# Performance work log

Measured on AMD Instinct MI355X. Metric: run time of the kernel, lower is better.

The kernel has to match this reference:

```python
import jax, jax.numpy as jnp
import numpy as np

H = 8            # num_heads
EPS = 1e-5       # LayerNorm eps (torch default)
SLOPE = 0.01     # leaky_relu negative slope (torch default)


def layernorm(x, g, b):
    mu = jnp.mean(x, axis=-1, keepdims=True)
    var = jnp.mean((x - mu) ** 2, axis=-1, keepdims=True)
    return (x - mu) * jax.lax.rsqrt(var + EPS) * g + b


def setup_inputs() -> dict:
    key = jax.random.key(0)
    ks = jax.random.split(key, 20)
    B, T, Din, Dh = 4, 2048, 512, 512
    s_in = 1.0 / np.sqrt(Din)
    s_h = 1.0 / np.sqrt(Dh)
    inp = {
        'q': jax.random.normal(ks[0], (B, T, Din), jnp.float32),
        'k': jax.random.normal(ks[1], (B, T, Din), jnp.float32),
        'v': jax.random.normal(ks[2], (B, T, Din), jnp.float32),
        # attention projections (stored as [in, out] for x @ W + b)
        'Wq': jax.random.uniform(ks[3], (Din, Dh), jnp.float32, -s_in, s_in),
        'bq': jax.random.uniform(ks[4], (Dh,), jnp.float32, -s_in, s_in),
        'Wk': jax.random.uniform(ks[5], (Din, Dh), jnp.float32, -s_in, s_in),
        'bk': jax.random.uniform(ks[6], (Dh,), jnp.float32, -s_in, s_in),
        'Wv': jax.random.uniform(ks[7], (Din, Dh), jnp.float32, -s_in, s_in),
        'bv': jax.random.uniform(ks[8], (Dh,), jnp.float32, -s_in, s_in),
        'Wo': jax.random.uniform(ks[9], (Dh, Dh), jnp.float32, -s_h, s_h),
        'bo': jax.random.uniform(ks[10], (Dh,), jnp.float32, -s_h, s_h),
        # FFN
        'Wh': jax.random.uniform(ks[11], (Dh, Dh), jnp.float32, -s_h, s_h),
        'bh': jax.random.uniform(ks[12], (Dh,), jnp.float32, -s_h, s_h),
        'W2': jax.random.uniform(ks[13], (Dh, Dh), jnp.float32, -s_h, s_h),
        'b2': jax.random.uniform(ks[14], (Dh,), jnp.float32, -s_h, s_h),
        # LayerNorms
        'g1': jnp.ones((Dh,), jnp.float32),
        'be1': jnp.zeros((Dh,), jnp.float32),
        'g2': jnp.ones((Dh,), jnp.float32),
        'be2': jnp.zeros((Dh,), jnp.float32),
    }
    return inp


def _block(q, k, v, Wq, bq, Wk, bk, Wv, bv, Wo, bo, Wh, bh, W2, b2, g1, be1, g2, be2):
    B, Tq, _ = q.shape
    Tk = k.shape[1]
    Dh = Wq.shape[1]
    dh = Dh // H
    # projections -> [B, H, T, dh]
    qh = (q @ Wq + bq).reshape(B, Tq, H, dh).transpose(0, 2, 1, 3)
    kh = (k @ Wk + bk).reshape(B, Tk, H, dh).transpose(0, 2, 1, 3)
    vh = (v @ Wv + bv).reshape(B, Tk, H, dh).transpose(0, 2, 1, 3)
    scores = jnp.einsum('bhqd,bhkd->bhqk', qh, kh) / np.sqrt(dh)
    # causal mask: tril with diagonal = Tk - Tq (matches get_causal_mask)
    mask = jnp.tril(jnp.ones((Tq, Tk), bool), k=Tk - Tq)
    scores = jnp.where(mask, scores, -jnp.inf)
    attn = jax.nn.softmax(scores, axis=-1)
    x = jnp.einsum('bhqk,bhkd->bhqd', attn, vh)
    x = x.transpose(0, 2, 1, 3).reshape(B, Tq, Dh)
    h = x @ Wo + bo
    if h.shape == q.shape:
        h = h + q  # residual
    h = layernorm(h, g1, be1)
    y = jax.nn.leaky_relu(h @ Wh + bh, SLOPE) @ W2 + b2
    y = y + h  # residual (shapes always equal here)
    return layernorm(y, g2, be2)


def reference(q, k, v, Wq, bq, Wk, bk, Wv, bv, Wo, bo, Wh, bh, W2, b2, g1, be1, g2, be2):
    return _block(q, k, v, Wq, bq, Wk, bk, Wv, bv, Wo, bo, Wh, bh, W2, b2, g1, be1, g2, be2)
```

## Files before the change

### kernel.cpp

```cpp
#include <hip/hip_runtime.h>
#include <math.h>

#define DIN   512
#define TSEQ  2048
#define BATCH 4
#define NH    8
#define DHEAD 64
#define MTOT  8192

typedef __attribute__((ext_vector_type(8))) __bf16 bf16x8;
typedef __attribute__((ext_vector_type(8))) short  s16x8;
typedef __attribute__((ext_vector_type(4))) float  f32x4;

__device__ __forceinline__ unsigned short f2b(float f) {
  union { float f; unsigned int u; } c; c.f = f;
  unsigned int r = (c.u + 0x7fffu + ((c.u >> 16) & 1u)) >> 16;
  return (unsigned short)r;
}

__device__ __forceinline__ float b2f(unsigned short u) {
  union { unsigned int i; float f; } c; c.i = (unsigned int)u << 16; return c.f;
}

__device__ __forceinline__ unsigned int pkbf(float a, float b) {
  union { __bf16 h[2]; unsigned int u; } c;
  c.h[0] = (__bf16)a; c.h[1] = (__bf16)b; return c.u;
}

__device__ __forceinline__ f32x4 mfma16(bf16x8 a, bf16x8 b, f32x4 c) {
  return __builtin_amdgcn_mfma_f32_16x16x32_bf16(a, b, c, 0, 0, 0);
}

__device__ __forceinline__ void gload16(const void* gsrc, void* ldsbase) {
  __builtin_amdgcn_global_load_lds(
      (const __attribute__((address_space(1))) unsigned int*)gsrc,
      (__attribute__((address_space(3))) unsigned int*)(unsigned int)(unsigned long long)ldsbase,
      16, 0, 0);
}

#define VMCNT0_BARRIER() do { \
    asm volatile("s_waitcnt vmcnt(0)" ::: "memory"); \
    __builtin_amdgcn_s_barrier(); } while (0)

__global__ __launch_bounds__(256) void cast3_kernel(const float* __restrict__ q,
                                                    const float* __restrict__ k,
                                                    const float* __restrict__ v,
                                                    unsigned short* __restrict__ oq,
                                                    unsigned short* __restrict__ ok,
                                                    unsigned short* __restrict__ ov) {
  const float* in = blockIdx.y == 0 ? q : blockIdx.y == 1 ? k : v;
  unsigned short* out = blockIdx.y == 0 ? oq : blockIdx.y == 1 ? ok : ov;
  int i = (blockIdx.x * 256 + threadIdx.x) * 8;
  float4 a = *(const float4*)(in + i);
  float4 b = *(const float4*)(in + i + 4);
  ushort4 u0, u1;
  u0.x = f2b(a.x); u0.y = f2b(a.y); u0.z = f2b(a.z); u0.w = f2b(a.w);
  u1.x = f2b(b.x); u1.y = f2b(b.y); u1.z = f2b(b.z); u1.w = f2b(b.w);
  *(ushort4*)(out + i) = u0;
  *(ushort4*)(out + i + 4) = u1;
}

__global__ __launch_bounds__(256) void transpose6_kernel(const float* __restrict__ w0,
                                                         const float* __restrict__ w1,
                                                         const float* __restrict__ w2,
                                                         const float* __restrict__ w3,
                                                         const float* __restrict__ w4,
                                                         const float* __restrict__ w5,
                                                         unsigned short* __restrict__ Wt) {
  const float* W;
  switch (blockIdx.z) {
    case 0: W = w0; break; case 1: W = w1; break; case 2: W = w2; break;
    case 3: W = w3; break; case 4: W = w4; break; default: W = w5; break;
  }
  unsigned short* dst = Wt + (size_t)blockIdx.z * 512 * 512;
  __shared__ float tile[32][33];
  int bx = blockIdx.x * 32, by = blockIdx.y * 32;
  int tx = threadIdx.x & 31, ty = threadIdx.x >> 5;
  #pragma unroll
  for (int yy = ty; yy < 32; yy += 8)
    tile[yy][tx] = W[(size_t)(by + yy) * DIN + bx + tx];
  __syncthreads();
  #pragma unroll
  for (int yy = ty; yy < 32; yy += 8)
    dst[(size_t)(bx + yy) * DIN + by + tx] = f2b(tile[tx][yy]);
}

__device__ __forceinline__ void gemm_core(const unsigned short* __restrict__ A,
                                          const unsigned short* __restrict__ Bt,
                                          int m0, int n0,
                                          unsigned short (*Als)[64 * 32],
                                          unsigned short (*Bls)[64 * 32],
                                          f32x4 (*acc)[2]) {
  const int tid = threadIdx.x, lane = tid & 63, w = tid >> 6;
  const int wr = w >> 1, wc = w & 1;
  const int l = lane & 15, g = lane >> 4;
  const int srow = lane >> 2;
  const int sce  = (lane & 3) * 8;

  #define GSTAGE(buf, k0) do { \
      gload16(A  + (size_t)(m0 + w * 16 + srow) * 512 + (k0) + sce, &Als[buf][w * 512]); \
      gload16(Bt + (size_t)(n0 + w * 16 + srow) * 512 + (k0) + sce, &Bls[buf][w * 512]); \
    } while (0)

  GSTAGE(0, 0);
  VMCNT0_BARRIER();
  for (int t = 0; t < 16; ++t) {
    int cur = t & 1;
    if (t < 15) GSTAGE(cur ^ 1, (t + 1) * 32);
    bf16x8 af[2], bf[2];
    #pragma unroll
    for (int m = 0; m < 2; ++m)
      af[m] = *(const bf16x8*)(&Als[cur][(wr * 32 + m * 16 + l) * 32 + g * 8]);
    #pragma unroll
    for (int n = 0; n < 2; ++n)
      bf[n] = *(const bf16x8*)(&Bls[cur][(wc * 32 + n * 16 + l) * 32 + g * 8]);
    #pragma unroll
    for (int m = 0; m < 2; ++m)
      #pragma unroll
      for (int n = 0; n < 2; ++n)
        acc[m][n] = mfma16(af[m], bf[n], acc[m][n]);
    VMCNT0_BARRIER();
  }
  #undef GSTAGE
}

enum { EPI_BF16 = 0, EPI_VT = 1, EPI_RESF32 = 2, EPI_RESB16 = 3, EPI_LRELU = 4 };

template <int EPI>
__global__ __launch_bounds__(256) void gemm_kernel(const unsigned short* __restrict__ A,
                                                   const unsigned short* __restrict__ Bt,
                                                   const float* __restrict__ bias,
                                                   const void* __restrict__ res,
                                                   unsigned short* __restrict__ out) {
  __shared__ unsigned short Als[2][64 * 32];
  __shared__ unsigned short Bls[2][64 * 32];
  const int lane = threadIdx.x & 63, w = threadIdx.x >> 6;
  const int wr = w >> 1, wc = w & 1;
  const int l = lane & 15, g = lane >> 4;
  const int m0 = blockIdx.x * 64, n0 = blockIdx.y * 64;
  f32x4 acc[2][2] = {};
  gemm_core(A, Bt, m0, n0, Als, Bls, acc);

  #pragma unroll
  for (int m = 0; m < 2; ++m) {
    int grb = m0 + wr * 32 + m * 16 + g * 4;
    #pragma unroll
    for (int n = 0; n < 2; ++n) {
      int gc = n0 + wc * 32 + n * 16 + l;
      float bv = bias[gc];
      #pragma unroll
      for (int r = 0; r < 4; ++r) {
        int gr = grb + r;
        float v = acc[m][n][r] + bv;
        if (EPI == EPI_RESF32) v += ((const float*)res)[(size_t)gr * 512 + gc];
        if (EPI == EPI_RESB16) v += b2f(((const unsigned short*)res)[(size_t)gr * 512 + gc]);
        if (EPI == EPI_LRELU)  v = v > 0.f ? v : 0.01f * v;
        if (EPI == EPI_VT) {
          int b = gr >> 11, t = gr & 2047;
          out[((size_t)(b * 512 + gc) << 11) + t] = f2b(v);
        } else {
          out[(size_t)gr * 512 + gc] = f2b(v);
        }
      }
    }
  }
}

__global__ __launch_bounds__(256) void gemm_qkv_kernel(const unsigned short* __restrict__ qb,
                                                       const unsigned short* __restrict__ kb,
                                                       const unsigned short* __restrict__ vb,
                                                       const unsigned short* __restrict__ Wt,
                                                       const float* __restrict__ bq,
                                                       const float* __restrict__ bk,
                                                       const float* __restrict__ bv,
                                                       unsigned short* __restrict__ Qp,
                                                       unsigned short* __restrict__ Kp,
                                                       unsigned short* __restrict__ Vt) {
  __shared__ unsigned short Als[2][64 * 32];
  __shared__ unsigned short Bls[2][64 * 32];
  const int z = blockIdx.z;
  const unsigned short* A = z == 0 ? qb : z == 1 ? kb : vb;
  const unsigned short* B = Wt + (size_t)z * 512 * 512;
  const float* bias = z == 0 ? bq : z == 1 ? bk : bv;
  const int lane = threadIdx.x & 63, w = threadIdx.x >> 6;
  const int wr = w >> 1, wc = w & 1;
  const int l = lane & 15, g = lane >> 4;
  const int m0 = blockIdx.x * 64, n0 = blockIdx.y * 64;
  f32x4 acc[2][2] = {};
  gemm_core(A, B, m0, n0, Als, Bls, acc);

  #pragma unroll
  for (int m = 0; m < 2; ++m) {
    int grb = m0 + wr * 32 + m * 16 + g * 4;
    #pragma unroll
    for (int n = 0; n < 2; ++n) {
      int gc = n0 + wc * 32 + n * 16 + l;
      float bvl = bias[gc];
      #pragma unroll
      for (int r = 0; r < 4; ++r) {
        int gr = grb + r;
        float v = acc[m][n][r] + bvl;
        if (z == 0) {
          Qp[(size_t)gr * 512 + gc] = f2b(v);
        } else if (z == 1) {
          Kp[(size_t)gr * 512 + gc] = f2b(v);
        } else {
          int b = gr >> 11, t = gr & 2047;
          Vt[((size_t)(b * 512 + gc) << 11) + t] = f2b(v);
        }
      }
    }
  }
}

__global__ __launch_bounds__(256) void attn_kernel(const unsigned short* __restrict__ Q,
                                                   const unsigned short* __restrict__ K,
                                                   const unsigned short* __restrict__ Vt,
                                                   unsigned short* __restrict__ O) {
  __shared__ unsigned short Kls[2][64 * 64];
  __shared__ unsigned short Pls[4][16 * 64];
  const int tid = threadIdx.x, lane = tid & 63, w = tid >> 6;
  const int l = lane & 15, g = lane >> 4;
  const int bh = blockIdx.x;
  const int qt = (int)gridDim.y - 1 - (int)blockIdx.y;
  const int b = bh >> 3, h = bh & 7;
  const int sx = (l & 7) * 8;
  const float SC2 = 0.125f * 1.44269504088896340736f;
  const float THR = 64.f;

  const int r8 = lane >> 3;
  const int sce = ((lane & 7) ^ r8) * 8;

  #define STAGEK(buf, kv0) do { \
      _Pragma("unroll") \
      for (int i_ = 0; i_ < 2; ++i_) { \
        int ii_ = w * 2 + i_; \
        gload16(K + (size_t)(b * 2048 + (kv0) + ii_ * 8 + r8) * 512 + h * 64 + sce, \
                &Kls[buf][ii_ * 512]); \
      } } while (0)

  const int q0 = qt * 64 + w * 16;
  bf16x8 qf[2];
  #pragma unroll
  for (int kf = 0; kf < 2; ++kf)
    qf[kf] = *(const bf16x8*)(Q + (size_t)(b * 2048 + q0 + l) * 512 + h * 64 + kf * 32 + g * 8);

  bf16x8 vones;
  #pragma unroll
  for (int i = 0; i < 8; ++i) vones[i] = (__bf16)1.0f;

  float mrun = -1e30f;
  f32x4 o[4] = {};
  f32x4 os = {0.f, 0.f, 0.f, 0.f};

  STAGEK(0, 0);
  VMCNT0_BARRIER();

  for (int s = 0; s <= qt; ++s) {
    int cur = s & 1;
    int kv0 = s * 64;
    if (s < qt) STAGEK(cur ^ 1, kv0 + 64);

    bf16x8 vf[2][4];
    #pragma unroll
    for (int kf = 0; kf < 2; ++kf)
      #pragma unroll
      for (int n = 0; n < 4; ++n)
        vf[kf][n] = *(const bf16x8*)(
            Vt + (size_t)(b * 512 + h * 64 + n * 16 + l) * 2048 + kv0 + kf * 32 + g * 8);

    f32x4 st[4];
    #pragma unroll
    for (int t = 0; t < 4; ++t) {
      st[t] = f32x4{0.f, 0.f, 0.f, 0.f};
      #pragma unroll
      for (int kf = 0; kf < 2; ++kf) {
        bf16x8 kfr = *(const bf16x8*)(&Kls[cur][(t * 16 + l) * 64 + ((kf * 32 + g * 8) ^ sx)]);
        st[t] = mfma16(kfr, qf[kf], st[t]);
      }
    }
    if (s == qt) {
      const int qrow = q0 + l;
      #pragma unroll
      for (int t = 0; t < 4; ++t)
        #pragma unroll
        for (int r = 0; r < 4; ++r)
          if (kv0 + t * 16 + g * 4 + r > qrow) st[t][r] = -1e30f;
    }

    float mx = fmaxf(
        fmaxf(fmaxf(fmaxf(st[0][0], st[0][1]), st[0][2]),
              fmaxf(fmaxf(st[0][3], st[1][0]), st[1][1])),
        fmaxf(fmaxf(fmaxf(st[1][2], st[1][3]), st[2][0]),
              fmaxf(fmaxf(st[2][1], st[2][2]), st[2][3])));
    mx = fmaxf(mx, fmaxf(fmaxf(st[3][0], st[3][1]), fmaxf(st[3][2], st[3][3])));
    mx = fmaxf(mx, __shfl_xor(mx, 16, 64));
    mx = fmaxf(mx, __shfl_xor(mx, 32, 64));

    if (!__all(mx <= mrun + THR)) {
      float nm = fmaxf(mrun, mx);
      float alpha = exp2f((mrun - nm) * SC2);
      mrun = nm;
      #pragma unroll
      for (int r = 0; r < 4; ++r) {
        float ar = __shfl(alpha, g * 4 + r, 64);
        #pragma unroll
        for (int n = 0; n < 4; ++n) o[n][r] *= ar;
        os[r] *= ar;
      }
    }

    float mS = mrun * SC2;
    #pragma unroll
    for (int t = 0; t < 4; ++t)
      #pragma unroll
      for (int r = 0; r < 4; ++r)
        st[t][r] = exp2f(fmaf(st[t][r], SC2, -mS));

    #pragma unroll
    for (int t = 0; t < 4; ++t) {
      uint2 u;
      u.x = pkbf(st[t][0], st[t][1]);
      u.y = pkbf(st[t][2], st[t][3]);
      *(uint2*)(&Pls[w][l * 64 + ((t * 16 + g * 4) ^ sx)]) = u;
    }
    #pragma unroll
    for (int kf = 0; kf < 2; ++kf) {
      bf16x8 pa = *(const bf16x8*)(&Pls[w][l * 64 + ((kf * 32 + g * 8) ^ sx)]);
      #pragma unroll
      for (int n = 0; n < 4; ++n)
        o[n] = mfma16(pa, vf[kf][n], o[n]);
      os = mfma16(pa, vones, os);
    }

    VMCNT0_BARRIER();
  }

  #pragma unroll
  for (int r = 0; r < 4; ++r) {
    float lir = 1.f / os[r];
    #pragma unroll
    for (int n = 0; n < 4; ++n)
      O[(size_t)(b * 2048 + q0 + g * 4 + r) * 512 + h * 64 + n * 16 + l] =
          f2b(o[n][r] * lir);
  }
  #undef STAGEK
}

template <int OUTF32>
__global__ __launch_bounds__(256) void lnb_kernel(const unsigned short* __restrict__ X,
                                                  const float* __restrict__ g,
                                                  const float* __restrict__ be,
                                                  float* __restrict__ Yf,
                                                  unsigned short* __restrict__ Yb) {
  int row = blockIdx.x * 4 + (threadIdx.x >> 6);
  int lane = threadIdx.x & 63;
  s16x8 v = *(const s16x8*)(X + (size_t)row * 512 + lane * 8);
  float f[8];
  #pragma unroll
  for (int j = 0; j < 8; ++j) f[j] = b2f((unsigned short)v[j]);
  float s = 0.f;
  #pragma unroll
  for (int j = 0; j < 8; ++j) s += f[j];
  #pragma unroll
  for (int t = 1; t < 64; t <<= 1) s += __shfl_xor(s, t, 64);
  float mu = s * (1.f / 512.f);
  float q = 0.f;
  #pragma unroll
  for (int j = 0; j < 8; ++j) q += (f[j] - mu) * (f[j] - mu);
  #pragma unroll
  for (int t = 1; t < 64; t <<= 1) q += __shfl_xor(q, t, 64);
  float rstd = rsqrtf(q * (1.f / 512.f) + 1e-5f);

  float4 g0 = *(const float4*)(g + lane * 8);
  float4 g1 = *(const float4*)(g + lane * 8 + 4);
  float4 b0 = *(const float4*)(be + lane * 8);
  float4 b1 = *(const float4*)(be + lane * 8 + 4);
  float y[8];
  y[0] = (f[0] - mu) * rstd * g0.x + b0.x; y[1] = (f[1] - mu) * rstd * g0.y + b0.y;
  y[2] = (f[2] - mu) * rstd * g0.z + b0.z; y[3] = (f[3] - mu) * rstd * g0.w + b0.w;
  y[4] = (f[4] - mu) * rstd * g1.x + b1.x; y[5] = (f[5] - mu) * rstd * g1.y + b1.y;
  y[6] = (f[6] - mu) * rstd * g1.z + b1.z; y[7] = (f[7] - mu) * rstd * g1.w + b1.w;
  if (OUTF32) {
    float4 o0 = {y[0], y[1], y[2], y[3]}, o1 = {y[4], y[5], y[6], y[7]};
    *(float4*)(Yf + (size_t)row * 512 + lane * 8) = o0;
    *(float4*)(Yf + (size_t)row * 512 + lane * 8 + 4) = o1;
  } else {
    uint4 u;
    u.x = pkbf(y[0], y[1]); u.y = pkbf(y[2], y[3]);
    u.z = pkbf(y[4], y[5]); u.w = pkbf(y[6], y[7]);
    *(uint4*)(Yb + (size_t)row * 512 + lane * 8) = u;
  }
}

extern "C" void kernel_launch(void* const* d_in, const int* in_sizes, int n_in,
                              void* d_out, int out_size, void* d_ws, size_t ws_size,
                              hipStream_t stream) {
  const float* q_in = (const float*)d_in[0];
  const float* k_in = (const float*)d_in[1];
  const float* v_in = (const float*)d_in[2];
  const float* Wq = (const float*)d_in[3];  const float* bq = (const float*)d_in[4];
  const float* Wk = (const float*)d_in[5];  const float* bk = (const float*)d_in[6];
  const float* Wv = (const float*)d_in[7];  const float* bv = (const float*)d_in[8];
  const float* Wo = (const float*)d_in[9];  const float* bo = (const float*)d_in[10];
  const float* Wh = (const float*)d_in[11]; const float* bh = (const float*)d_in[12];
  const float* W2 = (const float*)d_in[13]; const float* b2 = (const float*)d_in[14];
  const float* g1 = (const float*)d_in[15]; const float* be1 = (const float*)d_in[16];
  const float* g2 = (const float*)d_in[17]; const float* be2 = (const float*)d_in[18];

  char* ws = (char*)d_ws;
  const size_t MD2 = (size_t)MTOT * 512 * 2;
  const size_t W1  = (size_t)512 * 512 * 2;
  unsigned short* qb_  = (unsigned short*)(ws);
  unsigned short* kb_  = (unsigned short*)(ws + MD2);
  unsigned short* vb_  = (unsigned short*)(ws + 2 * MD2);
  unsigned short* Qp   = (unsigned short*)(ws + 3 * MD2);
  unsigned short* Kp   = (unsigned short*)(ws + 4 * MD2);
  unsigned short* Vt   = (unsigned short*)(ws + 5 * MD2);
  unsigned short* Wt   = (unsigned short*)(ws + 6 * MD2);
  unsigned short* attn = vb_;
  unsigned short* hy   = kb_;
  unsigned short* ln1b = qb_;
  unsigned short* f1   = Qp;
  unsigned short* y2   = Kp;

  cast3_kernel<<<dim3(MTOT * 512 / 2048, 3), 256, 0, stream>>>(q_in, k_in, v_in, qb_, kb_, vb_);
  transpose6_kernel<<<dim3(16, 16, 6), 256, 0, stream>>>(Wq, Wk, Wv, Wo, Wh, W2, Wt);

  gemm_qkv_kernel<<<dim3(MTOT / 64, 8, 3), 256, 0, stream>>>(
      qb_, kb_, vb_, Wt, bq, bk, bv, Qp, Kp, Vt);

  attn_kernel<<<dim3(BATCH * NH, 32), 256, 0, stream>>>(Qp, Kp, Vt, attn);

  dim3 gg(MTOT / 64, 8);
  gemm_kernel<EPI_RESF32><<<gg, 256, 0, stream>>>(attn, Wt + 3 * 512 * 512, bo, q_in, hy);
  lnb_kernel<0><<<MTOT / 4, 256, 0, stream>>>(hy, g1, be1, nullptr, ln1b);
  gemm_kernel<EPI_LRELU><<<gg, 256, 0, stream>>>(ln1b, Wt + 4 * 512 * 512, bh, nullptr, f1);
  gemm_kernel<EPI_RESB16><<<gg, 256, 0, stream>>>(f1, Wt + 5 * 512 * 512, b2, ln1b, y2);
  lnb_kernel<1><<<MTOT / 4, 256, 0, stream>>>(y2, g2, be2, (float*)d_out, nullptr);
}
```

Measured before the change: 297.0 us.

## Preload full B panel in LDS with 4-deep per-wave A pipeline; stage V via LDS

The GEMM core now loads the whole 64x512 B panel into LDS once, with an XOR swizzle. Each wave streams its own 16-row A slice through a 4-deep ring buffer using partial vmcnt waits instead of a block barrier every k-step. Each wave computes a 16x64 output tile in place of a 32x32 quadrant. In attention, V tiles are staged into LDS through async global-to-LDS loads alongside K, instead of being read directly from global memory into registers each iteration. This raises LDS use to about 80KB per GEMM block, which may lower occupancy, and removes the per-step barriers from the GEMM.

```diff
diff --git a/kernel.cpp b/kernel.cpp
--- a/kernel.cpp
+++ b/kernel.cpp
@@ -38,6 +38,7 @@
       16, 0, 0);
 }
 
+#define WAITV(N) asm volatile("s_waitcnt vmcnt(" #N ")" ::: "memory")
 #define VMCNT0_BARRIER() do { \
     asm volatile("s_waitcnt vmcnt(0)" ::: "memory"); \
     __builtin_amdgcn_s_barrier(); } while (0)
@@ -85,43 +86,48 @@
     dst[(size_t)(bx + yy) * DIN + by + tx] = f2b(tile[tx][yy]);
 }
 
-__device__ __forceinline__ void gemm_core(const unsigned short* __restrict__ A,
-                                          const unsigned short* __restrict__ Bt,
-                                          int m0, int n0,
-                                          unsigned short (*Als)[64 * 32],
-                                          unsigned short (*Bls)[64 * 32],
-                                          f32x4 (*acc)[2]) {
+__device__ __forceinline__ void gemm_core_ws(const unsigned short* __restrict__ A,
+                                             const unsigned short* __restrict__ Bt,
+                                             int m0, int n0,
+                                             unsigned short* __restrict__ Bls,
+                                             unsigned short* __restrict__ Alsw,
+                                             f32x4* __restrict__ acc) {
   const int tid = threadIdx.x, lane = tid & 63, w = tid >> 6;
-  const int wr = w >> 1, wc = w & 1;
   const int l = lane & 15, g = lane >> 4;
-  const int srow = lane >> 2;
-  const int sce  = (lane & 3) * 8;
-
-  #define GSTAGE(buf, k0) do { \
-      gload16(A  + (size_t)(m0 + w * 16 + srow) * 512 + (k0) + sce, &Als[buf][w * 512]); \
-      gload16(Bt + (size_t)(n0 + w * 16 + srow) * 512 + (k0) + sce, &Bls[buf][w * 512]); \
-    } while (0)
-
-  GSTAGE(0, 0);
-  VMCNT0_BARRIER();
+
+  #pragma unroll
+  for (int i = 0; i < 16; ++i) {
+    int row = w * 16 + i;
+    gload16(Bt + (size_t)(n0 + row) * 512 + ((lane ^ (row & 7)) * 8),
+            Bls + row * 512);
+  }
+
+  const int ar = lane >> 2;
+  const int ac = lane & 3;
+  const int asrc = (ac ^ ((ar >> 1) & 3)) * 8;
+  #define ASTAGE(buf, t) \
+    gload16(A + (size_t)(m0 + w * 16 + ar) * 512 + (t) * 32 + asrc, Alsw + (buf) * 512)
+
+  ASTAGE(0, 0); ASTAGE(1, 1); ASTAGE(2, 2);
+  WAITV(2);
+  __builtin_amdgcn_s_barrier();
+
+  const int aoff = l * 32 + (g ^ ((l >> 1) & 3)) * 8;
+  #pragma unroll
   for (int t = 0; t < 16; ++t) {
-    int cur = t & 1;
-    if (t < 15) GSTAGE(cur ^ 1, (t + 1) * 32);
-    bf16x8 af[2], bf[2];
-    #pragma unroll
-    for (int m = 0; m < 2; ++m)
-      af[m] = *(const bf16x8*)(&Als[cur][(wr * 32 + m * 16 + l) * 32 + g * 8]);
-    #pragma unroll
-    for (int n = 0; n < 2; ++n)
-      bf[n] = *(const bf16x8*)(&Bls[cur][(wc * 32 + n * 16 + l) * 32 + g * 8]);
-    #pragma unroll
-    for (int m = 0; m < 2; ++m)
-      #pragma unroll
-      for (int n = 0; n < 2; ++n)
-        acc[m][n] = mfma16(af[m], bf[n], acc[m][n]);
-    VMCNT0_BARRIER();
-  }
-  #undef GSTAGE
+    if (t + 3 < 16) ASTAGE((t + 3) & 3, t + 3);
+    if (t < 13) { WAITV(3); } else if (t == 13) { WAITV(2); }
+    else if (t == 14) { WAITV(1); } else { WAITV(0); }
+    bf16x8 af = *(const bf16x8*)(Alsw + (t & 3) * 512 + aoff);
+    #pragma unroll
+    for (int n = 0; n < 4; ++n) {
+      int row = n * 16 + l;
+      int ch = (t * 4 + g) ^ (l & 7);
+      bf16x8 bf = *(const bf16x8*)(Bls + row * 512 + ch * 8);
+      acc[n] = mfma16(af, bf, acc[n]);
+    }
+  }
+  #undef ASTAGE
 }
 
 enum { EPI_BF16 = 0, EPI_VT = 1, EPI_RESF32 = 2, EPI_RESB16 = 3, EPI_LRELU = 4 };
@@ -132,35 +138,31 @@
                                                    const float* __restrict__ bias,
                                                    const void* __restrict__ res,
                                                    unsigned short* __restrict__ out) {
-  __shared__ unsigned short Als[2][64 * 32];
-  __shared__ unsigned short Bls[2][64 * 32];
+  __shared__ unsigned short Bls[64 * 512];
+  __shared__ unsigned short Als[4][4][512];
   const int lane = threadIdx.x & 63, w = threadIdx.x >> 6;
-  const int wr = w >> 1, wc = w & 1;
   const int l = lane & 15, g = lane >> 4;
   const int m0 = blockIdx.x * 64, n0 = blockIdx.y * 64;
-  f32x4 acc[2][2] = {};
-  gemm_core(A, Bt, m0, n0, Als, Bls, acc);
-
-  #pragma unroll
-  for (int m = 0; m < 2; ++m) {
-    int grb = m0 + wr * 32 + m * 16 + g * 4;
-    #pragma unroll
-    for (int n = 0; n < 2; ++n) {
-      int gc = n0 + wc * 32 + n * 16 + l;
-      float bv = bias[gc];
-      #pragma unroll
-      for (int r = 0; r < 4; ++r) {
-        int gr = grb + r;
-        float v = acc[m][n][r] + bv;
-        if (EPI == EPI_RESF32) v += ((const float*)res)[(size_t)gr * 512 + gc];
-        if (EPI == EPI_RESB16) v += b2f(((const unsigned short*)res)[(size_t)gr * 512 + gc]);
-        if (EPI == EPI_LRELU)  v = v > 0.f ? v : 0.01f * v;
-        if (EPI == EPI_VT) {
-          int b = gr >> 11, t = gr & 2047;
-          out[((size_t)(b * 512 + gc) << 11) + t] = f2b(v);
-        } else {
-          out[(size_t)gr * 512 + gc] = f2b(v);
-        }
+  f32x4 acc[4] = {};
+  gemm_core_ws(A, Bt, m0, n0, Bls, &Als[w][0][0], acc);
+
+  int grb = m0 + w * 16 + g * 4;
+  #pragma unroll
+  for (int n = 0; n < 4; ++n) {
+    int gc = n0 + n * 16 + l;
+    float bv = bias[gc];
+    #pragma unroll
+    for (int r = 0; r < 4; ++r) {
+      int gr = grb + r;
+      float v = acc[n][r] + bv;
+      if (EPI == EPI_RESF32) v += ((const float*)res)[(size_t)gr * 512 + gc];
+      if (EPI == EPI_RESB16) v += b2f(((const unsigned short*)res)[(size_t)gr * 512 + gc]);
+      if (EPI == EPI_LRELU)  v = v > 0.f ? v : 0.01f * v;
+      if (EPI == EPI_VT) {
+        int b = gr >> 11, t = gr & 2047;
+        out[((size_t)(b * 512 + gc) << 11) + t] = f2b(v);
+      } else {
+        out[(size_t)gr * 512 + gc] = f2b(v);
       }
     }
   }
@@ -176,38 +178,34 @@
                                                        unsigned short* __restrict__ Qp,
                                                        unsigned short* __restrict__ Kp,
                                                        unsigned short* __restrict__ Vt) {
-  __shared__ unsigned short Als[2][64 * 32];
-  __shared__ unsigned short Bls[2][64 * 32];
+  __shared__ unsigned short Bls[64 * 512];
+  __shared__ unsigned short Als[4][4][512];
   const int z = blockIdx.z;
   const unsigned short* A = z == 0 ? qb : z == 1 ? kb : vb;
   const unsigned short* B = Wt + (size_t)z * 512 * 512;
   const float* bias = z == 0 ? bq : z == 1 ? bk : bv;
   const int lane = threadIdx.x & 63, w = threadIdx.x >> 6;
-  const int wr = w >> 1, wc = w & 1;
   const int l = lane & 15, g = lane >> 4;
   const int m0 = blockIdx.x * 64, n0 = blockIdx.y * 64;
-  f32x4 acc[2][2] = {};
-  gemm_core(A, B, m0, n0, Als, Bls, acc);
-
-  #pragma unroll
-  for (int m = 0; m < 2; ++m) {
-    int grb = m0 + wr * 32 + m * 16 + g * 4;
-    #pragma unroll
-    for (int n = 0; n < 2; ++n) {
-      int gc = n0 + wc * 32 + n * 16 + l;
-      float bvl = bias[gc];
-      #pragma unroll
-      for (int r = 0; r < 4; ++r) {
-        int gr = grb + r;
-        float v = acc[m][n][r] + bvl;
-        if (z == 0) {
-          Qp[(size_t)gr * 512 + gc] = f2b(v);
-        } else if (z == 1) {
-          Kp[(size_t)gr * 512 + gc] = f2b(v);
-        } else {
-          int b = gr >> 11, t = gr & 2047;
-          Vt[((size_t)(b * 512 + gc) << 11) + t] = f2b(v);
-        }
+  f32x4 acc[4] = {};
+  gemm_core_ws(A, B, m0, n0, Bls, &Als[w][0][0], acc);
+
+  int grb = m0 + w * 16 + g * 4;
+  #pragma unroll
+  for (int n = 0; n < 4; ++n) {
+    int gc = n0 + n * 16 + l;
+    float bvl = bias[gc];
+    #pragma unroll
+    for (int r = 0; r < 4; ++r) {
+      int gr = grb + r;
+      float v = acc[n][r] + bvl;
+      if (z == 0) {
+        Qp[(size_t)gr * 512 + gc] = f2b(v);
+      } else if (z == 1) {
+        Kp[(size_t)gr * 512 + gc] = f2b(v);
+      } else {
+        int b = gr >> 11, t = gr & 2047;
+        Vt[((size_t)(b * 512 + gc) << 11) + t] = f2b(v);
       }
     }
   }
@@ -218,6 +216,7 @@
                                                    const unsigned short* __restrict__ Vt,
                                                    unsigned short* __restrict__ O) {
   __shared__ unsigned short Kls[2][64 * 64];
+  __shared__ unsigned short Vls[2][64 * 64];
   __shared__ unsigned short Pls[4][16 * 64];
   const int tid = threadIdx.x, lane = tid & 63, w = tid >> 6;
   const int l = lane & 15, g = lane >> 4;
@@ -231,12 +230,13 @@
   const int r8 = lane >> 3;
   const int sce = ((lane & 7) ^ r8) * 8;
 
-  #define STAGEK(buf, kv0) do { \
+  #define STAGEKV(buf, kv0) do { \
       _Pragma("unroll") \
       for (int i_ = 0; i_ < 2; ++i_) { \
         int ii_ = w * 2 + i_; \
-        gload16(K + (size_t)(b * 2048 + (kv0) + ii_ * 8 + r8) * 512 + h * 64 + sce, \
-                &Kls[buf][ii_ * 512]); \
+        int row_ = ii_ * 8 + r8; \
+        gload16(K  + (size_t)(b * 2048 + (kv0) + row_) * 512 + h * 64 + sce, &Kls[buf][ii_ * 512]); \
+        gload16(Vt + (size_t)(b * 512 + h * 64 + row_) * 2048 + (kv0) + sce, &Vls[buf][ii_ * 512]); \
       } } while (0)
 
   const int q0 = qt * 64 + w * 16;
@@ -253,21 +253,13 @@
   f32x4 o[4] = {};
   f32x4 os = {0.f, 0.f, 0.f, 0.f};
 
-  STAGEK(0, 0);
+  STAGEKV(0, 0);
   VMCNT0_BARRIER();
 
   for (int s = 0; s <= qt; ++s) {
     int cur = s & 1;
     int kv0 = s * 64;
-    if (s < qt) STAGEK(cur ^ 1, kv0 + 64);
-
-    bf16x8 vf[2][4];
-    #pragma unroll
-    for (int kf = 0; kf < 2; ++kf)
-      #pragma unroll
-      for (int n = 0; n < 4; ++n)
-        vf[kf][n] = *(const bf16x8*)(
-            Vt + (size_t)(b * 512 + h * 64 + n * 16 + l) * 2048 + kv0 + kf * 32 + g * 8);
+    if (s < qt) STAGEKV(cur ^ 1, kv0 + 64);
 
     f32x4 st[4];
     #pragma unroll
@@ -328,8 +320,10 @@
     for (int kf = 0; kf < 2; ++kf) {
       bf16x8 pa = *(const bf16x8*)(&Pls[w][l * 64 + ((kf * 32 + g * 8) ^ sx)]);
       #pragma unroll
-      for (int n = 0; n < 4; ++n)
-        o[n] = mfma16(pa, vf[kf][n], o[n]);
+      for (int n = 0; n < 4; ++n) {
+        bf16x8 vf = *(const bf16x8*)(&Vls[cur][(n * 16 + l) * 64 + ((kf * 32 + g * 8) ^ sx)]);
+        o[n] = mfma16(pa, vf, o[n]);
+      }
       os = mfma16(pa, vones, os);
     }
 
@@ -344,7 +338,7 @@
       O[(size_t)(b * 2048 + q0 + g * 4 + r) * 512 + h * 64 + n * 16 + l] =
           f2b(o[n][r] * lir);
   }
-  #undef STAGEK
+  #undef STAGEKV
 }
 
 template <int OUTF32>
```

New measurement: 254.6 us. -14.3%, faster.

## Deepen GEMM LDS pipeline to four stages and stage V tiles via LDS

Applied to the files above, without the earlier changes.

The shared GEMM core moves from a two-buffer loop with a full vmcnt(0) wait each step to a four-buffer ring that prefetches three K-slices ahead and waits only on the oldest load with a partial vmcnt. This lets global loads overlap MFMA work across several iterations. The attention kernel now loads V tiles asynchronously into swizzled LDS alongside K, instead of having each lane issue direct global reads of V per iteration. Costs are double the LDS per GEMM block and an extra LDS buffer in attention, which may lower occupancy.

```diff
diff --git a/kernel.cpp b/kernel.cpp
--- a/kernel.cpp
+++ b/kernel.cpp
@@ -38,6 +38,7 @@
       16, 0, 0);
 }
 
+#define WAITV(N) asm volatile("s_waitcnt vmcnt(" #N ")" ::: "memory")
 #define VMCNT0_BARRIER() do { \
     asm volatile("s_waitcnt vmcnt(0)" ::: "memory"); \
     __builtin_amdgcn_s_barrier(); } while (0)
@@ -103,10 +104,14 @@
     } while (0)
 
   GSTAGE(0, 0);
-  VMCNT0_BARRIER();
+  GSTAGE(1, 32);
+  GSTAGE(2, 64);
+  #pragma unroll
   for (int t = 0; t < 16; ++t) {
-    int cur = t & 1;
-    if (t < 15) GSTAGE(cur ^ 1, (t + 1) * 32);
+    if (t < 14) { WAITV(4); } else if (t == 14) { WAITV(2); } else { WAITV(0); }
+    __builtin_amdgcn_s_barrier();
+    if (t + 3 < 16) GSTAGE((t + 3) & 3, (t + 3) * 32);
+    const int cur = t & 3;
     bf16x8 af[2], bf[2];
     #pragma unroll
     for (int m = 0; m < 2; ++m)
@@ -119,7 +124,6 @@
       #pragma unroll
       for (int n = 0; n < 2; ++n)
         acc[m][n] = mfma16(af[m], bf[n], acc[m][n]);
-    VMCNT0_BARRIER();
   }
   #undef GSTAGE
 }
@@ -132,8 +136,8 @@
                                                    const float* __restrict__ bias,
                                                    const void* __restrict__ res,
                                                    unsigned short* __restrict__ out) {
-  __shared__ unsigned short Als[2][64 * 32];
-  __shared__ unsigned short Bls[2][64 * 32];
+  __shared__ unsigned short Als[4][64 * 32];
+  __shared__ unsigned short Bls[4][64 * 32];
   const int lane = threadIdx.x & 63, w = threadIdx.x >> 6;
   const int wr = w >> 1, wc = w & 1;
   const int l = lane & 15, g = lane >> 4;
@@ -176,8 +180,8 @@
                                                        unsigned short* __restrict__ Qp,
                                                        unsigned short* __restrict__ Kp,
                                                        unsigned short* __restrict__ Vt) {
-  __shared__ unsigned short Als[2][64 * 32];
-  __shared__ unsigned short Bls[2][64 * 32];
+  __shared__ unsigned short Als[4][64 * 32];
+  __shared__ unsigned short Bls[4][64 * 32];
   const int z = blockIdx.z;
   const unsigned short* A = z == 0 ? qb : z == 1 ? kb : vb;
   const unsigned short* B = Wt + (size_t)z * 512 * 512;
@@ -218,6 +222,7 @@
                                                    const unsigned short* __restrict__ Vt,
                                                    unsigned short* __restrict__ O) {
   __shared__ unsigned short Kls[2][64 * 64];
+  __shared__ unsigned short Vls[2][64 * 64];
   __shared__ unsigned short Pls[4][16 * 64];
   const int tid = threadIdx.x, lane = tid & 63, w = tid >> 6;
   const int l = lane & 15, g = lane >> 4;
@@ -231,12 +236,13 @@
   const int r8 = lane >> 3;
   const int sce = ((lane & 7) ^ r8) * 8;
 
-  #define STAGEK(buf, kv0) do { \
+  #define STAGEKV(buf, kv0) do { \
       _Pragma("unroll") \
       for (int i_ = 0; i_ < 2; ++i_) { \
         int ii_ = w * 2 + i_; \
-        gload16(K + (size_t)(b * 2048 + (kv0) + ii_ * 8 + r8) * 512 + h * 64 + sce, \
-                &Kls[buf][ii_ * 512]); \
+        int row_ = ii_ * 8 + r8; \
+        gload16(K  + (size_t)(b * 2048 + (kv0) + row_) * 512 + h * 64 + sce, &Kls[buf][ii_ * 512]); \
+        gload16(Vt + (size_t)(b * 512 + h * 64 + row_) * 2048 + (kv0) + sce, &Vls[buf][ii_ * 512]); \
       } } while (0)
 
   const int q0 = qt * 64 + w * 16;
@@ -253,21 +259,13 @@
   f32x4 o[4] = {};
   f32x4 os = {0.f, 0.f, 0.f, 0.f};
 
-  STAGEK(0, 0);
+  STAGEKV(0, 0);
   VMCNT0_BARRIER();
 
   for (int s = 0; s <= qt; ++s) {
     int cur = s & 1;
     int kv0 = s * 64;
-    if (s < qt) STAGEK(cur ^ 1, kv0 + 64);
-
-    bf16x8 vf[2][4];
-    #pragma unroll
-    for (int kf = 0; kf < 2; ++kf)
-      #pragma unroll
-      for (int n = 0; n < 4; ++n)
-        vf[kf][n] = *(const bf16x8*)(
-            Vt + (size_t)(b * 512 + h * 64 + n * 16 + l) * 2048 + kv0 + kf * 32 + g * 8);
+    if (s < qt) STAGEKV(cur ^ 1, kv0 + 64);
 
     f32x4 st[4];
     #pragma unroll
@@ -328,8 +326,10 @@
     for (int kf = 0; kf < 2; ++kf) {
       bf16x8 pa = *(const bf16x8*)(&Pls[w][l * 64 + ((kf * 32 + g * 8) ^ sx)]);
       #pragma unroll
-      for (int n = 0; n < 4; ++n)
-        o[n] = mfma16(pa, vf[kf][n], o[n]);
+      for (int n = 0; n < 4; ++n) {
+        bf16x8 vf = *(const bf16x8*)(&Vls[cur][(n * 16 + l) * 64 + ((kf * 32 + g * 8) ^ sx)]);
+        o[n] = mfma16(pa, vf, o[n]);
+      }
       os = mfma16(pa, vones, os);
     }
 
@@ -344,7 +344,7 @@
       O[(size_t)(b * 2048 + q0 + g * 4 + r) * 512 + h * 64 + n * 16 + l] =
           f2b(o[n][r] * lir);
   }
-  #undef STAGEK
+  #undef STAGEKV
 }
 
 template <int OUTF32>
```

New measurement: 248.5 us. 16.3% less time.
